# Performance work log

Measured on AMD Instinct MI355X. Metric: run time of the kernel, lower is better.

## Reference

```python
import jax, jax.numpy as jnp
import numpy as np
from jax import lax

B, N, NCAM, NLVL = 2, 65536, 5, 3
CIN, MID, OUT, PTSC = 256, 128, 128, 128
H, W = 64, 112
EPS = 1e-3


def setup_inputs() -> dict:
    ks = jax.random.split(jax.random.key(0), 8)
    f32 = jnp.float32
    img_feats = jax.random.normal(ks[0], (NLVL, B * NCAM, CIN, H, W), f32)
    # points roughly in front of the cameras (z ~ 15) so many project in-bounds
    pts_xyz = jax.random.normal(ks[1], (B, N, 3), f32) * 10.0 + jnp.array([0.0, 0.0, 15.0], f32)
    cam_ids = jnp.sort(jax.random.randint(ks[2], (B, N), 0, NCAM), axis=1).astype(jnp.int32)
    pts_feats = jax.random.normal(ks[3], (B * N, PTSC), f32)
    T = jnp.broadcast_to(jnp.eye(4, dtype=f32), (NCAM, 4, 4))
    T = T.at[:, :3, 3].set(jax.random.normal(ks[4], (NCAM, 3), f32) * 0.5)
    fx, fy, cx, cy = 400.0, 400.0, 4.0 * W, 4.0 * H  # full-res intrinsics (feature stride 8)
    K = jnp.broadcast_to(jnp.array([[fx, 0.0, cx], [0.0, fy, cy], [0.0, 0.0, 1.0]], f32), (NCAM, 3, 3))
    conv_w = jax.random.normal(ks[5], (NLVL, MID, CIN, 3, 3), f32) * 0.02
    conv_b = jnp.zeros((NLVL, MID), f32)
    img_w = jax.random.normal(ks[6], (OUT, MID * NLVL), f32) * 0.05
    img_b = jnp.zeros((OUT,), f32)
    img_gamma = jnp.ones((OUT,), f32)
    img_beta = jnp.zeros((OUT,), f32)
    pts_w = jax.random.normal(ks[7], (OUT, PTSC), f32) * 0.05
    pts_b = jnp.zeros((OUT,), f32)
    pts_gamma = jnp.ones((OUT,), f32)
    pts_beta = jnp.zeros((OUT,), f32)
    return dict(img_feats=img_feats, pts_xyz=pts_xyz, pts_feats=pts_feats, T=T, K=K,
                conv_w=conv_w, conv_b=conv_b, img_w=img_w, img_b=img_b,
                img_gamma=img_gamma, img_beta=img_beta, pts_w=pts_w, pts_b=pts_b,
                pts_gamma=pts_gamma, pts_beta=pts_beta, cam_ids=cam_ids)


def _bn(x, gamma, beta):
    # BatchNorm1d in training mode: batch statistics, biased variance, eps=1e-3
    mu = jnp.mean(x, axis=0)
    var = jnp.var(x, axis=0)
    return (x - mu) * lax.rsqrt(var + EPS) * gamma + beta


def _bilinear(feat, bidx, cam, px, py):
    # feat: [B, NCAM, H, W, C]; px/py: [B, N] pixel coords (align_corners=True)
    # grid_sample bilinear with zeros padding: out-of-bounds corners contribute 0
    x0f = jnp.floor(px)
    y0f = jnp.floor(py)
    wx1 = px - x0f
    wy1 = py - y0f

    def corner(xf, yf, wgt):
        valid = (xf >= 0) & (xf <= W - 1) & (yf >= 0) & (yf <= H - 1)
        xi = jnp.clip(xf, 0, W - 1).astype(jnp.int32)
        yi = jnp.clip(yf, 0, H - 1).astype(jnp.int32)
        v = feat[bidx, cam, yi, xi]  # [B, N, C]
        return v * (wgt * valid)[..., None]

    return (corner(x0f, y0f, (1 - wx1) * (1 - wy1))
            + corner(x0f + 1, y0f, wx1 * (1 - wy1))
            + corner(x0f, y0f + 1, (1 - wx1) * wy1)
            + corner(x0f + 1, y0f + 1, wx1 * wy1))


def _forward(img_feats, pts_xyz, pts_feats, T, K, conv_w, conv_b, img_w, img_b,
             img_gamma, img_beta, pts_w, pts_b, pts_gamma, pts_beta, cam_ids):
    # scale intrinsics to the 1/8-resolution feature maps (K[0,0],K[0,2],K[1,1],K[1,2] /= 8)
    k_scale = jnp.array([[0.125, 1.0, 0.125], [1.0, 0.125, 0.125], [1.0, 1.0, 1.0]], jnp.float32)
    Ks = K * k_scale
    ones = jnp.ones(pts_xyz.shape[:2] + (1,), pts_xyz.dtype)
    xyz1 = jnp.concatenate([pts_xyz, ones], axis=-1)      # [B, N, 4]
    Tc = T[cam_ids]                                        # [B, N, 4, 4]
    Kc = Ks[cam_ids]                                       # [B, N, 3, 3]
    pc = jnp.einsum('bnij,bnj->bni', Tc, xyz1)[..., :3]    # camera-frame coords
    pim = jnp.einsum('bnij,bnj->bni', Kc, pc)
    uv = pim[..., :2] / pim[..., 2:3]
    gx = uv[..., 0] / W * 2.0 - 1.0                        # normalized grid coords
    gy = uv[..., 1] / H * 2.0 - 1.0
    px = (gx + 1.0) * 0.5 * (W - 1)                        # align_corners=True mapping
    py = (gy + 1.0) * 0.5 * (H - 1)
    bidx = jnp.broadcast_to(jnp.arange(B)[:, None], cam_ids.shape)
    lvl_feats = []
    for l in range(NLVL):
        f = lax.conv_general_dilated(img_feats[l], conv_w[l], (1, 1), 'SAME',
                                     dimension_numbers=('NCHW', 'OIHW', 'NCHW'))
        f = f + conv_b[l][None, :, None, None]
        f = f.reshape(B, NCAM, MID, H, W).transpose(0, 1, 3, 4, 2)  # [B,NCAM,H,W,C]
        lvl_feats.append(_bilinear(f, bidx, cam_ids, px, py))       # [B,N,MID]
    img_pts = jnp.concatenate(lvl_feats, axis=-1).reshape(B * N, MID * NLVL)
    img_pre = _bn(img_pts @ img_w.T + img_b, img_gamma, img_beta)
    pts_pre = _bn(pts_feats @ pts_w.T + pts_b, pts_gamma, pts_beta)
    return jax.nn.relu(img_pre + pts_pre)


def reference(img_feats, pts_xyz, pts_feats, T, K, conv_w, conv_b, img_w, img_b,
              img_gamma, img_beta, pts_w, pts_b, pts_gamma, pts_beta, cam_ids):
    return _forward(img_feats, pts_xyz, pts_feats, T, K, conv_w, conv_b, img_w, img_b,
                    img_gamma, img_beta, pts_w, pts_b, pts_gamma, pts_beta, cam_ids)
```

## Files before the change

kernel.cpp:

```cpp
#include <hip/hip_runtime.h>
#include <cstdint>

#define LVLPOS 75240
#define GUARD  256
#define NPOST  75264

using f32x4  = __attribute__((ext_vector_type(4))) float;
using bf16x8 = __attribute__((ext_vector_type(8))) __bf16;

static __device__ __forceinline__ unsigned short f2bf(float f) {
  unsigned int u = __float_as_uint(f);
  u += 0x7fffu + ((u >> 16) & 1u);
  return (unsigned short)(u >> 16);
}
static __device__ __forceinline__ float bflo(uint32_t d) { return __uint_as_float(d << 16); }
static __device__ __forceinline__ float bfhi(uint32_t d) { return __uint_as_float(d & 0xffff0000u); }

#if __has_builtin(__builtin_amdgcn_global_load_lds)
#define HAVE_GLL 1
typedef const __attribute__((address_space(1))) unsigned int* gas1_t;
typedef __attribute__((address_space(3))) unsigned int* las3_t;
static __device__ __forceinline__ void gll16(const void* g, void* l) {
  __builtin_amdgcn_global_load_lds((gas1_t)g, (las3_t)l, 16, 0, 0);
}
#else
#define HAVE_GLL 0
#endif

#define OFF_WF     ((size_t)0)
#define OFF_BIAS   ((size_t)1769472)
#define OFF_PTSWB  ((size_t)1769984)
#define OFF_STATS  ((size_t)1802752)
#define OFF_FDAT   ((size_t)1804800)
#define OFF_IMGP   ((size_t)21072384)
#define OFF_IRAW   OFF_IMGP
#define OFF_PRAW   (OFF_IMGP + (size_t)33554432)

__global__ __launch_bounds__(256) void k_zero(unsigned short* __restrict__ imgP) {
  const int b = blockIdx.x, t = threadIdx.x;
  size_t base; int n16;
  if (b == 0)      { base = 0;                          n16 = 8192; }
  else if (b == 1) { base = (size_t)(GUARD + 3 * LVLPOS) * 256; n16 = 8192; }
  else {
    int z = b - 2, lvl = z / 20, w = z % 20, n = w >> 1, y = (w & 1) ? 65 : 0;
    base = (size_t)(GUARD + lvl * LVLPOS + (n * 66 + y) * 114) * 256;
    n16 = 3648;
  }
  uint4 zz = {0u, 0u, 0u, 0u};
  uint4* d = (uint4*)(imgP + base);
  for (int v = t; v < n16; v += 256) d[v] = zz;
}

__global__ __launch_bounds__(256) void k_fold_w(const float* __restrict__ img_w,
                                                const float* __restrict__ conv_w,
                                                unsigned short* __restrict__ wf) {
  __shared__ float iw[128 * 130];
  __shared__ float cw[128 * 33];
  const int bid = blockIdx.x;
  const int l = bid / 72, r = bid % 72, tap = r / 8, ckk = r % 8;
  const int t = threadIdx.x;
  for (int v = t; v < 4096; v += 256) {
    int o = v >> 5, seg = v & 31;
    float4 f = *(const float4*)(img_w + o * 384 + l * 128 + seg * 4);
    float* d = iw + o * 130 + seg * 4;
    d[0] = f.x; d[1] = f.y; d[2] = f.z; d[3] = f.w;
  }
  for (int v = t; v < 4096; v += 256) {
    int mid = v >> 5, cj = v & 31;
    cw[mid * 33 + cj] = conv_w[(size_t)(((l * 128 + mid) * 256) + (ckk * 32 + cj)) * 9 + tap];
  }
  __syncthreads();
  const int o = t & 127, cs = t >> 7;
  float accs[16];
  #pragma unroll
  for (int ci = 0; ci < 16; ++ci) accs[ci] = 0.f;
  for (int mid = 0; mid < 128; ++mid) {
    float a = iw[o * 130 + mid];
    #pragma unroll
    for (int ci = 0; ci < 16; ++ci) accs[ci] = fmaf(a, cw[mid * 33 + cs * 16 + ci], accs[ci]);
  }
  const int nt = o >> 4;
  #pragma unroll
  for (int ci = 0; ci < 16; ++ci) {
    int c = ckk * 32 + cs * 16 + ci;
    int ck64 = c >> 6, c64 = c & 63;
    int kh = c64 >> 5, kq3 = (c64 >> 3) & 3, el = c64 & 7;
    int lane = (o & 15) + (kq3 << 4);
    size_t idx = (size_t)((l * 4 + ck64) * 9 + tap) * 8192
               + (size_t)((nt * 2 + kh) * 512) + lane * 8 + el;
    wf[idx] = f2bf(accs[ci]);
  }
}

__global__ __launch_bounds__(256) void k_misc(const float* __restrict__ img_w,
                                              const float* __restrict__ conv_b,
                                              const float* __restrict__ pts_w,
                                              float* __restrict__ bias,
                                              unsigned short* __restrict__ pts_wb) {
  const int t = threadIdx.x;
  if (blockIdx.x == 0) {
    if (t < 128) {
      float a = 0.f;
      for (int i = 0; i < 384; ++i) a = fmaf(img_w[t * 384 + i], conv_b[i], a);
      bias[t] = a;
    }
  } else {
    int idx = (blockIdx.x - 1) * 256 + t;
    pts_wb[idx] = f2bf(pts_w[idx]);
  }
}

__global__ __launch_bounds__(256) void k_nhwc(const float* __restrict__ img,
                                              unsigned short* __restrict__ imgP) {
  __shared__ unsigned short tile[256 * 114];
  const int t = threadIdx.x;
  const int lvl = blockIdx.x / 640, r = blockIdx.x % 640, n = r >> 6, y = r & 63;
  const float4* src4 = (const float4*)(img + (size_t)(lvl * 10 + n) * 1835008 + (size_t)y * 112);
  for (int v = t; v < 7168; v += 256) {
    int c = v / 28, s = v - c * 28;
    float4 f = src4[(size_t)c * 1792 + s];
    uint2 d;
    d.x = (uint32_t)f2bf(f.x) | ((uint32_t)f2bf(f.y) << 16);
    d.y = (uint32_t)f2bf(f.z) | ((uint32_t)f2bf(f.w) << 16);
    *(uint2*)(tile + c * 114 + s * 4) = d;
  }
  __syncthreads();
  uint32_t* dst = (uint32_t*)(imgP + (size_t)(GUARD + lvl * LVLPOS + (n * 66 + y + 1) * 114) * 256);
  for (int v = t; v < 14592; v += 256) {
    int xp = v >> 7, cp = v & 127;
    uint32_t val = 0;
    if (xp >= 1 && xp <= 112) {
      int x = xp - 1;
      val = (uint32_t)tile[(2 * cp) * 114 + x] | ((uint32_t)tile[(2 * cp + 1) * 114 + x] << 16);
    }
    dst[v] = val;
  }
}

__global__ __launch_bounds__(256, 3) void k_conv(const unsigned short* __restrict__ imgP,
                                                 const unsigned short* __restrict__ wf,
                                                 const float* __restrict__ bias,
                                                 unsigned short* __restrict__ fdat) {
  __shared__ unsigned short lds[9360 + 2 * 8192];
  unsigned short* As = lds;
  unsigned short* Bs = lds + 9360;
  const int t = threadIdx.x, lane = t & 63, wave = t >> 6;
  const int mh = wave & 1, nh = wave >> 1;
  const int m = lane & 15, kq = lane >> 4;
  const int m0 = blockIdx.x * 128;

  f32x4 acc[4][4];
  #pragma unroll
  for (int i = 0; i < 4; ++i)
    #pragma unroll
    for (int j = 0; j < 4; ++j) acc[i][j] = (f32x4){0.f, 0.f, 0.f, 0.f};

  for (int lvl = 0; lvl < 3; ++lvl) {
    const unsigned short* Alvl = imgP + ((size_t)GUARD + (size_t)lvl * LVLPOS + m0 - 1) * 256;
    for (int ck = 0; ck < 4; ++ck) {
      for (int ky = 0; ky < 3; ++ky) {
        const unsigned short* Asrc = Alvl + (ptrdiff_t)(ky - 1) * 114 * 256 + ck * 64;
        for (int v = t; v < 1040; v += 256) {
          int p = v >> 3, seg = v & 7;
          uint4 d = *(const uint4*)(Asrc + (size_t)p * 256 + seg * 8);
          *(uint4*)(As + p * 72 + seg * 8) = d;
        }
        const unsigned short* Bsrc = wf + (size_t)((lvl * 4 + ck) * 9 + ky * 3) * 8192;
#if HAVE_GLL
        #pragma unroll
        for (int i = 0; i < 4; ++i) {
          int chunk = wave * 4 + i;
          gll16(Bsrc + chunk * 512 + lane * 8, Bs + chunk * 512);
        }
#else
        for (int v = t; v < 1024; v += 256)
          *(uint4*)(Bs + v * 8) = *(const uint4*)(Bsrc + v * 8);
#endif
        __syncthreads();
        #pragma unroll
        for (int kx = 0; kx < 3; ++kx) {
          if (kx < 2) {
            const unsigned short* Bn = Bsrc + (kx + 1) * 8192;
            unsigned short* Bd = Bs + ((kx + 1) & 1) * 8192;
#if HAVE_GLL
            #pragma unroll
            for (int i = 0; i < 4; ++i) {
              int chunk = wave * 4 + i;
              gll16(Bn + chunk * 512 + lane * 8, Bd + chunk * 512);
            }
#else
            for (int v = t; v < 1024; v += 256)
              *(uint4*)(Bd + v * 8) = *(const uint4*)(Bn + v * 8);
#endif
          }
          const unsigned short* Bb = Bs + (kx & 1) * 8192;
          bf16x8 bfr[4][2];
          #pragma unroll
          for (int nt = 0; nt < 4; ++nt) {
            const unsigned short* bp = Bb + ((nh * 4 + nt) * 2) * 512 + lane * 8;
            bfr[nt][0] = *(const bf16x8*)(bp);
            bfr[nt][1] = *(const bf16x8*)(bp + 512);
          }
          #pragma unroll
          for (int mt = 0; mt < 4; ++mt) {
            const unsigned short* ap = As + (mh * 64 + mt * 16 + m + kx) * 72 + kq * 8;
            bf16x8 a0 = *(const bf16x8*)(ap);
            bf16x8 a1 = *(const bf16x8*)(ap + 32);
            #pragma unroll
            for (int nt = 0; nt < 4; ++nt) {
              acc[mt][nt] = __builtin_amdgcn_mfma_f32_16x16x32_bf16(a0, bfr[nt][0], acc[mt][nt], 0, 0, 0);
              acc[mt][nt] = __builtin_amdgcn_mfma_f32_16x16x32_bf16(a1, bfr[nt][1], acc[mt][nt], 0, 0, 0);
            }
          }
          __syncthreads();
        }
      }
    }
  }

  unsigned short* Ep = lds;
  #pragma unroll
  for (int nt = 0; nt < 4; ++nt) {
    int oc = nh * 64 + nt * 16 + m;
    float bv = bias[oc];
    #pragma unroll
    for (int mt = 0; mt < 4; ++mt)
      #pragma unroll
      for (int rr = 0; rr < 4; ++rr)
        Ep[(mh * 64 + mt * 16 + kq * 4 + rr) * 128 + oc] = f2bf(acc[mt][nt][rr] + bv);
  }
  __syncthreads();
  unsigned short* dst = fdat + (size_t)m0 * 128;
  for (int v = t; v < 2048; v += 256)
    *(uint4*)(dst + v * 8) = *(const uint4*)(Ep + v * 8);
}

__global__ __launch_bounds__(256) void k_gather(const float* __restrict__ pts_xyz,
                                                const int* __restrict__ cam_ids,
                                                const float* __restrict__ Tm,
                                                const float* __restrict__ Km,
                                                const unsigned short* __restrict__ fdat,
                                                unsigned short* __restrict__ img_raw) {
  const int t = threadIdx.x, lane = t & 63, wave = t >> 6;
  const int p0 = blockIdx.x * 16 + wave * 4;
  const uint32_t* fq = (const uint32_t*)fdat;
  for (int j = 0; j < 4; ++j) {
    const int p = p0 + j;
    const int b = p >> 16;
    const int cam = cam_ids[p];
    const float X = pts_xyz[(size_t)p * 3], Y = pts_xyz[(size_t)p * 3 + 1], Z = pts_xyz[(size_t)p * 3 + 2];
    const float* Tc = Tm + cam * 16;
    float pcx = Tc[0] * X + Tc[1] * Y + Tc[2]  * Z + Tc[3];
    float pcy = Tc[4] * X + Tc[5] * Y + Tc[6]  * Z + Tc[7];
    float pcz = Tc[8] * X + Tc[9] * Y + Tc[10] * Z + Tc[11];
    const float* Kc = Km + cam * 9;
    float pimx = Kc[0] * 0.125f * pcx + Kc[1] * pcy          + Kc[2] * 0.125f * pcz;
    float pimy = Kc[3] * pcx          + Kc[4] * 0.125f * pcy + Kc[5] * 0.125f * pcz;
    float pimz = Kc[6] * pcx          + Kc[7] * pcy          + Kc[8] * pcz;
    float u = pimx / pimz, vv = pimy / pimz;
    float px = (u / 112.f) * 111.f;
    float py = (vv / 64.f) * 63.f;
    float x0 = floorf(px), y0 = floorf(py);
    float wx = px - x0, wy = py - y0;
    float cxf[4] = {x0, x0 + 1.f, x0, x0 + 1.f};
    float cyf[4] = {y0, y0, y0 + 1.f, y0 + 1.f};
    float cwt[4] = {(1.f - wx) * (1.f - wy), wx * (1.f - wy), (1.f - wx) * wy, wx * wy};
    const int nimg = b * 5 + cam;
    float wv[4]; int idx[4]; bool any = false;
    #pragma unroll
    for (int c4 = 0; c4 < 4; ++c4) {
      float xf = cxf[c4], yf = cyf[c4];
      bool valid = (xf >= 0.f) && (xf <= 111.f) && (yf >= 0.f) && (yf <= 63.f);
      float w = cwt[c4] * (valid ? 1.f : 0.f);
      int xi = (int)fminf(fmaxf(xf, 0.f), 111.f);
      int yi = (int)fminf(fmaxf(yf, 0.f), 63.f);
      wv[c4] = w;
      idx[c4] = (nimg * 66 + yi + 1) * 114 + xi + 1;
      any = any || (w != 0.f);
    }
    float acc0 = 0.f, acc1 = 0.f;
    if (any) {
      #pragma unroll
      for (int c4 = 0; c4 < 4; ++c4) {
        uint32_t d = fq[(size_t)idx[c4] * 64 + lane];
        acc0 = fmaf(wv[c4], bflo(d), acc0);
        acc1 = fmaf(wv[c4], bfhi(d), acc1);
      }
    }
    ((uint32_t*)img_raw)[(size_t)p * 64 + lane] =
        (uint32_t)f2bf(acc0) | ((uint32_t)f2bf(acc1) << 16);
  }
}

#define PP 136
__global__ __launch_bounds__(256, 2) void k_ptsgemm(const float* __restrict__ pts_feats,
                                                    const unsigned short* __restrict__ pts_wb,
                                                    unsigned short* __restrict__ pts_raw) {
  __shared__ unsigned short Asm[128 * PP];
  __shared__ unsigned short Bsm[128 * PP];
  const int t = threadIdx.x, lane = t & 63, wave = t >> 6;
  const int mh = wave & 1, nh = wave >> 1;
  const int m = lane & 15, kq = lane >> 4;
  const size_t r0 = (size_t)blockIdx.x * 128;
  for (int v = t; v < 2048; v += 256) {
    int o = v >> 4, seg = v & 15;
    *(uint4*)(Bsm + o * PP + seg * 8) = *(const uint4*)(pts_wb + o * 128 + seg * 8);
  }
  for (int v = t; v < 4096; v += 256) {
    int mm = v >> 5, seg = v & 31;
    float4 f = *(const float4*)(pts_feats + (r0 + mm) * 128 + seg * 4);
    uint2 d;
    d.x = (uint32_t)f2bf(f.x) | ((uint32_t)f2bf(f.y) << 16);
    d.y = (uint32_t)f2bf(f.z) | ((uint32_t)f2bf(f.w) << 16);
    *(uint2*)(Asm + mm * PP + seg * 4) = d;
  }
  __syncthreads();
  f32x4 acc[4][4];
  #pragma unroll
  for (int i = 0; i < 4; ++i)
    #pragma unroll
    for (int jj = 0; jj < 4; ++jj) acc[i][jj] = (f32x4){0.f, 0.f, 0.f, 0.f};
  #pragma unroll
  for (int ks = 0; ks < 4; ++ks) {
    bf16x8 bfr[4];
    #pragma unroll
    for (int nt = 0; nt < 4; ++nt)
      bfr[nt] = *(const bf16x8*)(Bsm + (nh * 64 + nt * 16 + m) * PP + ks * 32 + kq * 8);
    #pragma unroll
    for (int mt = 0; mt < 4; ++mt) {
      bf16x8 af = *(const bf16x8*)(Asm + (mh * 64 + mt * 16 + m) * PP + ks * 32 + kq * 8);
      #pragma unroll
      for (int nt = 0; nt < 4; ++nt)
        acc[mt][nt] = __builtin_amdgcn_mfma_f32_16x16x32_bf16(af, bfr[nt], acc[mt][nt], 0, 0, 0);
    }
  }
  __syncthreads();
  #pragma unroll
  for (int mt = 0; mt < 4; ++mt)
    #pragma unroll
    for (int nt = 0; nt < 4; ++nt)
      #pragma unroll
      for (int rr = 0; rr < 4; ++rr)
        Asm[(mh * 64 + mt * 16 + kq * 4 + rr) * 128 + nh * 64 + nt * 16 + m] = f2bf(acc[mt][nt][rr]);
  __syncthreads();
  unsigned short* dst = pts_raw + r0 * 128;
  for (int v = t; v < 2048; v += 256)
    *(uint4*)(dst + v * 8) = *(const uint4*)(Asm + v * 8);
}

__global__ __launch_bounds__(256) void k_stats(const unsigned short* __restrict__ img_raw,
                                               const unsigned short* __restrict__ pts_raw,
                                               float* __restrict__ stats) {
  const int bid = blockIdx.x;
  const uint32_t* src = (const uint32_t*)((bid < 256) ? img_raw : pts_raw);
  const int blk = bid & 255;
  const int t = threadIdx.x, cp = t & 63, rg = t >> 6;
  float s0 = 0.f, q0 = 0.f, s1 = 0.f, q1 = 0.f;
  for (int i = 0; i < 128; ++i) {
    int row = blk * 512 + rg * 128 + i;
    uint32_t d = src[(size_t)row * 64 + cp];
    float v0 = bflo(d), v1 = bfhi(d);
    s0 += v0; q0 += v0 * v0; s1 += v1; q1 += v1 * v1;
  }
  const int base = (bid < 256) ? 0 : 256;
  atomicAdd(&stats[base + 2 * cp], s0);
  atomicAdd(&stats[base + 2 * cp + 1], s1);
  atomicAdd(&stats[base + 128 + 2 * cp], q0);
  atomicAdd(&stats[base + 128 + 2 * cp + 1], q1);
}

__global__ __launch_bounds__(256) void k_final(const unsigned short* __restrict__ img_raw,
                                               const unsigned short* __restrict__ pts_raw,
                                               const float* __restrict__ stats,
                                               const float* __restrict__ img_gamma,
                                               const float* __restrict__ img_beta,
                                               const float* __restrict__ pts_gamma,
                                               const float* __restrict__ pts_beta,
                                               float* __restrict__ out) {
  __shared__ float sA[128], sB[128], sC[128];
  const int t = threadIdx.x;
  if (t < 128) {
    const float Nr = 131072.f;
    float mu_i = stats[t] / Nr;
    float var_i = stats[128 + t] / Nr - mu_i * mu_i;
    float a_i = img_gamma[t] * rsqrtf(var_i + 1e-3f);
    float mu_p = stats[256 + t] / Nr;
    float var_p = stats[384 + t] / Nr - mu_p * mu_p;
    float a_p = pts_gamma[t] * rsqrtf(var_p + 1e-3f);
    sA[t] = a_i; sB[t] = a_p;
    sC[t] = img_beta[t] + pts_beta[t] - a_i * mu_i - a_p * mu_p;
  }
  __syncthreads();
  const uint32_t* ir = (const uint32_t*)img_raw;
  const uint32_t* pr = (const uint32_t*)pts_raw;
  size_t g0 = (size_t)blockIdx.x * 2048;
  for (int i = 0; i < 8; ++i) {
    size_t g = g0 + i * 256 + t;
    uint32_t di = ir[g], dp = pr[g];
    int c = (int)(g & 63) * 2;
    float o0 = fmaxf(0.f, sA[c] * bflo(di) + sB[c] * bflo(dp) + sC[c]);
    float o1 = fmaxf(0.f, sA[c + 1] * bfhi(di) + sB[c + 1] * bfhi(dp) + sC[c + 1]);
    float2 o; o.x = o0; o.y = o1;
    *(float2*)(out + g * 2) = o;
  }
}

extern "C" void kernel_launch(void* const* d_in, const int* in_sizes, int n_in,
                              void* d_out, int out_size, void* d_ws, size_t ws_size,
                              hipStream_t stream) {
  const float* img_feats = (const float*)d_in[0];
  const float* pts_xyz   = (const float*)d_in[1];
  const float* pts_feats = (const float*)d_in[2];
  const float* Tm        = (const float*)d_in[3];
  const float* Km        = (const float*)d_in[4];
  const float* conv_w    = (const float*)d_in[5];
  const float* conv_b    = (const float*)d_in[6];
  const float* img_w     = (const float*)d_in[7];
  const float* img_gamma = (const float*)d_in[9];
  const float* img_beta  = (const float*)d_in[10];
  const float* pts_w     = (const float*)d_in[11];
  const float* pts_gamma = (const float*)d_in[13];
  const float* pts_beta  = (const float*)d_in[14];
  const int*   cam_ids   = (const int*)d_in[15];

  char* wsb = (char*)d_ws;
  unsigned short* wf      = (unsigned short*)(wsb + OFF_WF);
  float*          bias    = (float*)(wsb + OFF_BIAS);
  unsigned short* pts_wb  = (unsigned short*)(wsb + OFF_PTSWB);
  float*          stats   = (float*)(wsb + OFF_STATS);
  unsigned short* fdat    = (unsigned short*)(wsb + OFF_FDAT);
  unsigned short* imgP    = (unsigned short*)(wsb + OFF_IMGP);
  unsigned short* img_raw = (unsigned short*)(wsb + OFF_IRAW);
  unsigned short* pts_raw = (unsigned short*)(wsb + OFF_PRAW);

  hipMemsetAsync(stats, 0, 2048, stream);
  k_zero<<<dim3(62), dim3(256), 0, stream>>>(imgP);
  k_fold_w<<<dim3(216), dim3(256), 0, stream>>>(img_w, conv_w, wf);
  k_misc<<<dim3(65), dim3(256), 0, stream>>>(img_w, conv_b, pts_w, bias, pts_wb);

  k_nhwc<<<dim3(1920), dim3(256), 0, stream>>>(img_feats, imgP);
  k_conv<<<dim3(588), dim3(256), 0, stream>>>(imgP, wf, bias, fdat);

  k_gather<<<dim3(8192), dim3(256), 0, stream>>>(pts_xyz, cam_ids, Tm, Km, fdat, img_raw);
  k_ptsgemm<<<dim3(1024), dim3(256), 0, stream>>>(pts_feats, pts_wb, pts_raw);
  k_stats<<<dim3(512), dim3(256), 0, stream>>>(img_raw, pts_raw, stats);
  k_final<<<dim3(4096), dim3(256), 0, stream>>>(img_raw, pts_raw, stats,
                                                img_gamma, img_beta, pts_gamma, pts_beta,
                                                (float*)d_out);
}
```

Measured before the change: 753.9 us.

## Merge setup kernels, retile conv, fuse gather with pts GEMM and stats

```diff
diff --git a/kernel.cpp b/kernel.cpp
--- a/kernel.cpp
+++ b/kernel.cpp
@@ -3,7 +3,7 @@
 
 #define LVLPOS 75240
 #define GUARD  256
-#define NPOST  75264
+#define NPART  16
 
 using f32x4  = __attribute__((ext_vector_type(4))) float;
 using bf16x8 = __attribute__((ext_vector_type(8))) __bf16;
@@ -16,97 +16,90 @@
 static __device__ __forceinline__ float bflo(uint32_t d) { return __uint_as_float(d << 16); }
 static __device__ __forceinline__ float bfhi(uint32_t d) { return __uint_as_float(d & 0xffff0000u); }
 
-#if __has_builtin(__builtin_amdgcn_global_load_lds)
-#define HAVE_GLL 1
-typedef const __attribute__((address_space(1))) unsigned int* gas1_t;
-typedef __attribute__((address_space(3))) unsigned int* las3_t;
-static __device__ __forceinline__ void gll16(const void* g, void* l) {
-  __builtin_amdgcn_global_load_lds((gas1_t)g, (las3_t)l, 16, 0, 0);
-}
-#else
-#define HAVE_GLL 0
-#endif
-
 #define OFF_WF     ((size_t)0)
 #define OFF_BIAS   ((size_t)1769472)
 #define OFF_PTSWB  ((size_t)1769984)
-#define OFF_STATS  ((size_t)1802752)
-#define OFF_FDAT   ((size_t)1804800)
-#define OFF_IMGP   ((size_t)21072384)
+#define OFF_STATSP ((size_t)1802752)
+#define OFF_FDAT   ((size_t)1835520)
+#define OFF_IMGP   ((size_t)21103104)
 #define OFF_IRAW   OFF_IMGP
 #define OFF_PRAW   (OFF_IMGP + (size_t)33554432)
 
-__global__ __launch_bounds__(256) void k_zero(unsigned short* __restrict__ imgP) {
+__global__ __launch_bounds__(256) void k_setup(const float* __restrict__ img_w,
+                                               const float* __restrict__ conv_w,
+                                               const float* __restrict__ conv_b,
+                                               const float* __restrict__ pts_w,
+                                               unsigned short* __restrict__ wf,
+                                               float* __restrict__ bias,
+                                               unsigned short* __restrict__ pts_wb,
+                                               unsigned short* __restrict__ imgP,
+                                               float* __restrict__ statsP) {
+  __shared__ float smem[12544];
   const int b = blockIdx.x, t = threadIdx.x;
-  size_t base; int n16;
-  if (b == 0)      { base = 0;                          n16 = 8192; }
-  else if (b == 1) { base = (size_t)(GUARD + 3 * LVLPOS) * 256; n16 = 8192; }
-  else {
-    int z = b - 2, lvl = z / 20, w = z % 20, n = w >> 1, y = (w & 1) ? 65 : 0;
-    base = (size_t)(GUARD + lvl * LVLPOS + (n * 66 + y) * 114) * 256;
-    n16 = 3648;
-  }
-  uint4 zz = {0u, 0u, 0u, 0u};
-  uint4* d = (uint4*)(imgP + base);
-  for (int v = t; v < n16; v += 256) d[v] = zz;
-}
-
-__global__ __launch_bounds__(256) void k_fold_w(const float* __restrict__ img_w,
-                                                const float* __restrict__ conv_w,
-                                                unsigned short* __restrict__ wf) {
-  __shared__ float iw[128 * 130];
-  __shared__ float cw[128 * 33];
-  const int bid = blockIdx.x;
-  const int l = bid / 72, r = bid % 72, tap = r / 8, ckk = r % 8;
-  const int t = threadIdx.x;
-  for (int v = t; v < 4096; v += 256) {
-    int o = v >> 5, seg = v & 31;
-    float4 f = *(const float4*)(img_w + o * 384 + l * 128 + seg * 4);
-    float* d = iw + o * 130 + seg * 4;
-    d[0] = f.x; d[1] = f.y; d[2] = f.z; d[3] = f.w;
-  }
-  for (int v = t; v < 4096; v += 256) {
-    int mid = v >> 5, cj = v & 31;
-    cw[mid * 33 + cj] = conv_w[(size_t)(((l * 128 + mid) * 256) + (ckk * 32 + cj)) * 9 + tap];
-  }
-  __syncthreads();
-  const int o = t & 127, cs = t >> 7;
-  float accs[16];
-  #pragma unroll
-  for (int ci = 0; ci < 16; ++ci) accs[ci] = 0.f;
-  for (int mid = 0; mid < 128; ++mid) {
-    float a = iw[o * 130 + mid];
-    #pragma unroll
-    for (int ci = 0; ci < 16; ++ci) accs[ci] = fmaf(a, cw[mid * 33 + cs * 16 + ci], accs[ci]);
-  }
-  const int nt = o >> 4;
-  #pragma unroll
-  for (int ci = 0; ci < 16; ++ci) {
-    int c = ckk * 32 + cs * 16 + ci;
-    int ck64 = c >> 6, c64 = c & 63;
-    int kh = c64 >> 5, kq3 = (c64 >> 3) & 3, el = c64 & 7;
-    int lane = (o & 15) + (kq3 << 4);
-    size_t idx = (size_t)((l * 4 + ck64) * 9 + tap) * 8192
-               + (size_t)((nt * 2 + kh) * 512) + lane * 8 + el;
-    wf[idx] = f2bf(accs[ci]);
-  }
-}
-
-__global__ __launch_bounds__(256) void k_misc(const float* __restrict__ img_w,
-                                              const float* __restrict__ conv_b,
-                                              const float* __restrict__ pts_w,
-                                              float* __restrict__ bias,
-                                              unsigned short* __restrict__ pts_wb) {
-  const int t = threadIdx.x;
-  if (blockIdx.x == 0) {
-    if (t < 128) {
-      float a = 0.f;
-      for (int i = 0; i < 384; ++i) a = fmaf(img_w[t * 384 + i], conv_b[i], a);
-      bias[t] = a;
+  if (b < 432) {
+    int z = b >> 1, oh = b & 1;
+    int l = z / 72, r = z % 72, tap = r / 8, ckk = r % 8;
+    float* iw = smem;
+    float* cw = smem + 8320;
+    for (int v = t; v < 2048; v += 256) {
+      int o = v >> 5, seg = v & 31;
+      float4 f = *(const float4*)(img_w + (size_t)(oh * 64 + o) * 384 + l * 128 + seg * 4);
+      float* d = iw + o * 130 + seg * 4;
+      d[0] = f.x; d[1] = f.y; d[2] = f.z; d[3] = f.w;
+    }
+    for (int v = t; v < 4096; v += 256) {
+      int mid = v >> 5, cj = v & 31;
+      cw[mid * 33 + cj] = conv_w[(size_t)((l * 128 + mid) * 256 + ckk * 32 + cj) * 9 + tap];
+    }
+    __syncthreads();
+    const int o64 = t & 63, cs = t >> 6, o = oh * 64 + o64;
+    float accs[8];
+    #pragma unroll
+    for (int ci = 0; ci < 8; ++ci) accs[ci] = 0.f;
+    for (int mid = 0; mid < 128; ++mid) {
+      float a = iw[o64 * 130 + mid];
+      #pragma unroll
+      for (int ci = 0; ci < 8; ++ci) accs[ci] = fmaf(a, cw[mid * 33 + cs * 8 + ci], accs[ci]);
+    }
+    #pragma unroll
+    for (int ci = 0; ci < 8; ++ci) {
+      int c = ckk * 32 + cs * 8 + ci;
+      int ck64 = c >> 6, c64 = c & 63;
+      int kh = c64 >> 5, kq3 = (c64 >> 3) & 3, el = c64 & 7;
+      size_t idx = (size_t)((l * 4 + ck64) * 9 + tap) * 8192
+                 + (size_t)(((o >> 4) * 2 + kh) * 512) + ((o & 15) + 16 * kq3) * 8 + el;
+      wf[idx] = f2bf(accs[ci]);
+    }
+  } else if (b < 494) {
+    int z = b - 432;
+    size_t base; int n16;
+    if (z == 60)      { base = 0; n16 = 8192; }
+    else if (z == 61) { base = (size_t)(GUARD + 3 * LVLPOS) * 256; n16 = 8192; }
+    else {
+      int lvl = z / 20, w = z % 20, n = w >> 1, y = (w & 1) ? 65 : 0;
+      base = (size_t)(GUARD + lvl * LVLPOS + (n * 66 + y) * 114) * 256; n16 = 3648;
+    }
+    uint4 zz = {0u, 0u, 0u, 0u};
+    uint4* d = (uint4*)(imgP + base);
+    for (int v = t; v < n16; v += 256) d[v] = zz;
+  } else if (b < 559) {
+    int z = b - 494;
+    if (z == 0) {
+      if (t < 128) {
+        float a = 0.f;
+        for (int i = 0; i < 384; ++i) a = fmaf(img_w[t * 384 + i], conv_b[i], a);
+        bias[t] = a;
+      }
+    } else {
+      int idx = (z - 1) * 256 + t;
+      int o = idx >> 7, k = idx & 127;
+      int ks = k >> 5, kq = (k >> 3) & 3, el = k & 7;
+      int pos = (ks * 8 + (o >> 4)) * 512 + ((o & 15) + 16 * kq) * 8 + el;
+      pts_wb[pos] = f2bf(pts_w[idx]);
     }
   } else {
-    int idx = (blockIdx.x - 1) * 256 + t;
-    pts_wb[idx] = f2bf(pts_w[idx]);
+    int z = b - 559;
+    ((float4*)statsP)[z * 256 + t] = (float4){0.f, 0.f, 0.f, 0.f};
   }
 }
 
@@ -137,241 +130,242 @@
   }
 }
 
-__global__ __launch_bounds__(256, 3) void k_conv(const unsigned short* __restrict__ imgP,
+#define APITCH 72
+static __device__ __forceinline__ void conv_stage(unsigned short* dst,
+                                                  const unsigned short* __restrict__ imgP,
+                                                  int s, int m0, int t) {
+  int lvl = s / 12, r = s - lvl * 12;
+  int ck = r / 3, ky = r - ck * 3;
+  const unsigned short* base = imgP
+      + (size_t)(GUARD + lvl * LVLPOS + m0 - 1 + (ky - 1) * 114) * 256 + ck * 64;
+  for (int v = t; v < 528; v += 256) {
+    int p = v >> 3, seg = v & 7;
+    *(uint4*)(dst + p * APITCH + seg * 8) = *(const uint4*)(base + (size_t)p * 256 + seg * 8);
+  }
+}
+
+static __device__ __forceinline__ void conv_compute(const unsigned short* As_,
+                                                    const unsigned short* __restrict__ wf,
+                                                    int s, int mh, int nh, int m, int kq,
+                                                    f32x4 (&acc)[2][4]) {
+  const unsigned short* W0 = wf + (size_t)(3 * s) * 8192 + (nh * 8) * 512 + (m + 16 * kq) * 8;
+  #pragma unroll
+  for (int kx = 0; kx < 3; ++kx) {
+    const unsigned short* Wp = W0 + kx * 8192;
+    bf16x8 bv[4][2];
+    #pragma unroll
+    for (int nt = 0; nt < 4; ++nt) {
+      bv[nt][0] = *(const bf16x8*)(Wp + (nt * 2) * 512);
+      bv[nt][1] = *(const bf16x8*)(Wp + (nt * 2 + 1) * 512);
+    }
+    #pragma unroll
+    for (int mt = 0; mt < 2; ++mt) {
+      const unsigned short* ap = As_ + (mh * 32 + mt * 16 + m + kx) * APITCH + kq * 8;
+      bf16x8 a0 = *(const bf16x8*)(ap);
+      bf16x8 a1 = *(const bf16x8*)(ap + 32);
+      #pragma unroll
+      for (int nt = 0; nt < 4; ++nt) {
+        acc[mt][nt] = __builtin_amdgcn_mfma_f32_16x16x32_bf16(a0, bv[nt][0], acc[mt][nt], 0, 0, 0);
+        acc[mt][nt] = __builtin_amdgcn_mfma_f32_16x16x32_bf16(a1, bv[nt][1], acc[mt][nt], 0, 0, 0);
+      }
+    }
+  }
+}
+
+__global__ __launch_bounds__(256, 4) void k_conv(const unsigned short* __restrict__ imgP,
                                                  const unsigned short* __restrict__ wf,
                                                  const float* __restrict__ bias,
                                                  unsigned short* __restrict__ fdat) {
-  __shared__ unsigned short lds[9360 + 2 * 8192];
-  unsigned short* As = lds;
-  unsigned short* Bs = lds + 9360;
+  __shared__ unsigned short As[2][66 * APITCH];
   const int t = threadIdx.x, lane = t & 63, wave = t >> 6;
   const int mh = wave & 1, nh = wave >> 1;
   const int m = lane & 15, kq = lane >> 4;
-  const int m0 = blockIdx.x * 128;
-
-  f32x4 acc[4][4];
+  const int m0 = blockIdx.x * 64;
+
+  f32x4 acc[2][4];
   #pragma unroll
-  for (int i = 0; i < 4; ++i)
+  for (int i = 0; i < 2; ++i)
     #pragma unroll
     for (int j = 0; j < 4; ++j) acc[i][j] = (f32x4){0.f, 0.f, 0.f, 0.f};
 
-  for (int lvl = 0; lvl < 3; ++lvl) {
-    const unsigned short* Alvl = imgP + ((size_t)GUARD + (size_t)lvl * LVLPOS + m0 - 1) * 256;
-    for (int ck = 0; ck < 4; ++ck) {
-      for (int ky = 0; ky < 3; ++ky) {
-        const unsigned short* Asrc = Alvl + (ptrdiff_t)(ky - 1) * 114 * 256 + ck * 64;
-        for (int v = t; v < 1040; v += 256) {
-          int p = v >> 3, seg = v & 7;
-          uint4 d = *(const uint4*)(Asrc + (size_t)p * 256 + seg * 8);
-          *(uint4*)(As + p * 72 + seg * 8) = d;
-        }
-        const unsigned short* Bsrc = wf + (size_t)((lvl * 4 + ck) * 9 + ky * 3) * 8192;
-#if HAVE_GLL
-        #pragma unroll
-        for (int i = 0; i < 4; ++i) {
-          int chunk = wave * 4 + i;
-          gll16(Bsrc + chunk * 512 + lane * 8, Bs + chunk * 512);
-        }
-#else
-        for (int v = t; v < 1024; v += 256)
-          *(uint4*)(Bs + v * 8) = *(const uint4*)(Bsrc + v * 8);
-#endif
-        __syncthreads();
-        #pragma unroll
-        for (int kx = 0; kx < 3; ++kx) {
-          if (kx < 2) {
-            const unsigned short* Bn = Bsrc + (kx + 1) * 8192;
-            unsigned short* Bd = Bs + ((kx + 1) & 1) * 8192;
-#if HAVE_GLL
-            #pragma unroll
-            for (int i = 0; i < 4; ++i) {
-              int chunk = wave * 4 + i;
-              gll16(Bn + chunk * 512 + lane * 8, Bd + chunk * 512);
-            }
-#else
-            for (int v = t; v < 1024; v += 256)
-              *(uint4*)(Bd + v * 8) = *(const uint4*)(Bn + v * 8);
-#endif
-          }
-          const unsigned short* Bb = Bs + (kx & 1) * 8192;
-          bf16x8 bfr[4][2];
-          #pragma unroll
-          for (int nt = 0; nt < 4; ++nt) {
-            const unsigned short* bp = Bb + ((nh * 4 + nt) * 2) * 512 + lane * 8;
-            bfr[nt][0] = *(const bf16x8*)(bp);
-            bfr[nt][1] = *(const bf16x8*)(bp + 512);
-          }
-          #pragma unroll
-          for (int mt = 0; mt < 4; ++mt) {
-            const unsigned short* ap = As + (mh * 64 + mt * 16 + m + kx) * 72 + kq * 8;
-            bf16x8 a0 = *(const bf16x8*)(ap);
-            bf16x8 a1 = *(const bf16x8*)(ap + 32);
-            #pragma unroll
-            for (int nt = 0; nt < 4; ++nt) {
-              acc[mt][nt] = __builtin_amdgcn_mfma_f32_16x16x32_bf16(a0, bfr[nt][0], acc[mt][nt], 0, 0, 0);
-              acc[mt][nt] = __builtin_amdgcn_mfma_f32_16x16x32_bf16(a1, bfr[nt][1], acc[mt][nt], 0, 0, 0);
-            }
-          }
-          __syncthreads();
-        }
-      }
-    }
-  }
-
-  unsigned short* Ep = lds;
+  conv_stage(As[0], imgP, 0, m0, t);
+  #pragma unroll 1
+  for (int s = 0; s < 36; s += 2) {
+    __syncthreads();
+    if (s + 1 < 36) conv_stage(As[1], imgP, s + 1, m0, t);
+    conv_compute(As[0], wf, s, mh, nh, m, kq, acc);
+    __syncthreads();
+    if (s + 2 < 36) conv_stage(As[0], imgP, s + 2, m0, t);
+    conv_compute(As[1], wf, s + 1, mh, nh, m, kq, acc);
+  }
+  __syncthreads();
+
+  unsigned short* Ep = &As[0][0];
   #pragma unroll
   for (int nt = 0; nt < 4; ++nt) {
     int oc = nh * 64 + nt * 16 + m;
     float bv = bias[oc];
     #pragma unroll
-    for (int mt = 0; mt < 4; ++mt)
+    for (int mt = 0; mt < 2; ++mt)
       #pragma unroll
       for (int rr = 0; rr < 4; ++rr)
-        Ep[(mh * 64 + mt * 16 + kq * 4 + rr) * 128 + oc] = f2bf(acc[mt][nt][rr] + bv);
+        Ep[(mh * 32 + mt * 16 + kq * 4 + rr) * 128 + oc] = f2bf(acc[mt][nt][rr] + bv);
   }
   __syncthreads();
   unsigned short* dst = fdat + (size_t)m0 * 128;
-  for (int v = t; v < 2048; v += 256)
+  for (int v = t; v < 1024; v += 256)
     *(uint4*)(dst + v * 8) = *(const uint4*)(Ep + v * 8);
 }
 
-__global__ __launch_bounds__(256) void k_gather(const float* __restrict__ pts_xyz,
-                                                const int* __restrict__ cam_ids,
-                                                const float* __restrict__ Tm,
-                                                const float* __restrict__ Km,
-                                                const unsigned short* __restrict__ fdat,
-                                                unsigned short* __restrict__ img_raw) {
+__global__ __launch_bounds__(256) void k_gp(const float* __restrict__ pts_xyz,
+                                            const int* __restrict__ cam_ids,
+                                            const float* __restrict__ Tm,
+                                            const float* __restrict__ Km,
+                                            const unsigned short* __restrict__ fdat,
+                                            const float* __restrict__ pts_feats,
+                                            const unsigned short* __restrict__ pts_wb,
+                                            unsigned short* __restrict__ img_raw,
+                                            unsigned short* __restrict__ pts_raw,
+                                            float* __restrict__ statsP) {
+  __shared__ __align__(16) char smem[36864];
   const int t = threadIdx.x, lane = t & 63, wave = t >> 6;
-  const int p0 = blockIdx.x * 16 + wave * 4;
-  const uint32_t* fq = (const uint32_t*)fdat;
-  for (int j = 0; j < 4; ++j) {
-    const int p = p0 + j;
-    const int b = p >> 16;
-    const int cam = cam_ids[p];
-    const float X = pts_xyz[(size_t)p * 3], Y = pts_xyz[(size_t)p * 3 + 1], Z = pts_xyz[(size_t)p * 3 + 2];
-    const float* Tc = Tm + cam * 16;
-    float pcx = Tc[0] * X + Tc[1] * Y + Tc[2]  * Z + Tc[3];
-    float pcy = Tc[4] * X + Tc[5] * Y + Tc[6]  * Z + Tc[7];
-    float pcz = Tc[8] * X + Tc[9] * Y + Tc[10] * Z + Tc[11];
-    const float* Kc = Km + cam * 9;
-    float pimx = Kc[0] * 0.125f * pcx + Kc[1] * pcy          + Kc[2] * 0.125f * pcz;
-    float pimy = Kc[3] * pcx          + Kc[4] * 0.125f * pcy + Kc[5] * 0.125f * pcz;
-    float pimz = Kc[6] * pcx          + Kc[7] * pcy          + Kc[8] * pcz;
-    float u = pimx / pimz, vv = pimy / pimz;
-    float px = (u / 112.f) * 111.f;
-    float py = (vv / 64.f) * 63.f;
-    float x0 = floorf(px), y0 = floorf(py);
-    float wx = px - x0, wy = py - y0;
-    float cxf[4] = {x0, x0 + 1.f, x0, x0 + 1.f};
-    float cyf[4] = {y0, y0, y0 + 1.f, y0 + 1.f};
-    float cwt[4] = {(1.f - wx) * (1.f - wy), wx * (1.f - wy), (1.f - wx) * wy, wx * wy};
-    const int nimg = b * 5 + cam;
-    float wv[4]; int idx[4]; bool any = false;
-    #pragma unroll
-    for (int c4 = 0; c4 < 4; ++c4) {
-      float xf = cxf[c4], yf = cyf[c4];
-      bool valid = (xf >= 0.f) && (xf <= 111.f) && (yf >= 0.f) && (yf <= 63.f);
-      float w = cwt[c4] * (valid ? 1.f : 0.f);
-      int xi = (int)fminf(fmaxf(xf, 0.f), 111.f);
-      int yi = (int)fminf(fmaxf(yf, 0.f), 63.f);
-      wv[c4] = w;
-      idx[c4] = (nimg * 66 + yi + 1) * 114 + xi + 1;
-      any = any || (w != 0.f);
-    }
-    float acc0 = 0.f, acc1 = 0.f;
-    if (any) {
+
+  if (blockIdx.x < 8192) {
+    float* sb = (float*)smem;
+    float* qb = sb + 128;
+    if (t < 128) { sb[t] = 0.f; sb[128 + t] = 0.f; }
+    __syncthreads();
+    const int p0 = blockIdx.x * 16 + wave * 4;
+    const uint32_t* fq = (const uint32_t*)fdat;
+    float s0 = 0.f, q0 = 0.f, s1 = 0.f, q1 = 0.f;
+    for (int j = 0; j < 4; ++j) {
+      const int p = p0 + j;
+      const int b = p >> 16;
+      const int cam = cam_ids[p];
+      const float X = pts_xyz[(size_t)p * 3], Y = pts_xyz[(size_t)p * 3 + 1], Z = pts_xyz[(size_t)p * 3 + 2];
+      const float* Tc = Tm + cam * 16;
+      float pcx = Tc[0] * X + Tc[1] * Y + Tc[2]  * Z + Tc[3];
+      float pcy = Tc[4] * X + Tc[5] * Y + Tc[6]  * Z + Tc[7];
+      float pcz = Tc[8] * X + Tc[9] * Y + Tc[10] * Z + Tc[11];
+      const float* Kc = Km + cam * 9;
+      float pimx = Kc[0] * 0.125f * pcx + Kc[1] * pcy          + Kc[2] * 0.125f * pcz;
+      float pimy = Kc[3] * pcx          + Kc[4] * 0.125f * pcy + Kc[5] * 0.125f * pcz;
+      float pimz = Kc[6] * pcx          + Kc[7] * pcy          + Kc[8] * pcz;
+      float u = pimx / pimz, vv = pimy / pimz;
+      float px = (u / 112.f) * 111.f;
+      float py = (vv / 64.f) * 63.f;
+      float x0 = floorf(px), y0 = floorf(py);
+      float wx = px - x0, wy = py - y0;
+      float cxf[4] = {x0, x0 + 1.f, x0, x0 + 1.f};
+      float cyf[4] = {y0, y0, y0 + 1.f, y0 + 1.f};
+      float cwt[4] = {(1.f - wx) * (1.f - wy), wx * (1.f - wy), (1.f - wx) * wy, wx * wy};
+      const int nimg = b * 5 + cam;
+      float wv[4]; int idx[4]; bool any = false;
       #pragma unroll
       for (int c4 = 0; c4 < 4; ++c4) {
-        uint32_t d = fq[(size_t)idx[c4] * 64 + lane];
-        acc0 = fmaf(wv[c4], bflo(d), acc0);
-        acc1 = fmaf(wv[c4], bfhi(d), acc1);
-      }
-    }
-    ((uint32_t*)img_raw)[(size_t)p * 64 + lane] =
-        (uint32_t)f2bf(acc0) | ((uint32_t)f2bf(acc1) << 16);
-  }
-}
-
-#define PP 136
-__global__ __launch_bounds__(256, 2) void k_ptsgemm(const float* __restrict__ pts_feats,
-                                                    const unsigned short* __restrict__ pts_wb,
-                                                    unsigned short* __restrict__ pts_raw) {
-  __shared__ unsigned short Asm[128 * PP];
-  __shared__ unsigned short Bsm[128 * PP];
-  const int t = threadIdx.x, lane = t & 63, wave = t >> 6;
-  const int mh = wave & 1, nh = wave >> 1;
-  const int m = lane & 15, kq = lane >> 4;
-  const size_t r0 = (size_t)blockIdx.x * 128;
-  for (int v = t; v < 2048; v += 256) {
-    int o = v >> 4, seg = v & 15;
-    *(uint4*)(Bsm + o * PP + seg * 8) = *(const uint4*)(pts_wb + o * 128 + seg * 8);
-  }
-  for (int v = t; v < 4096; v += 256) {
-    int mm = v >> 5, seg = v & 31;
-    float4 f = *(const float4*)(pts_feats + (r0 + mm) * 128 + seg * 4);
-    uint2 d;
-    d.x = (uint32_t)f2bf(f.x) | ((uint32_t)f2bf(f.y) << 16);
-    d.y = (uint32_t)f2bf(f.z) | ((uint32_t)f2bf(f.w) << 16);
-    *(uint2*)(Asm + mm * PP + seg * 4) = d;
-  }
-  __syncthreads();
-  f32x4 acc[4][4];
-  #pragma unroll
-  for (int i = 0; i < 4; ++i)
-    #pragma unroll
-    for (int jj = 0; jj < 4; ++jj) acc[i][jj] = (f32x4){0.f, 0.f, 0.f, 0.f};
-  #pragma unroll
-  for (int ks = 0; ks < 4; ++ks) {
-    bf16x8 bfr[4];
-    #pragma unroll
-    for (int nt = 0; nt < 4; ++nt)
-      bfr[nt] = *(const bf16x8*)(Bsm + (nh * 64 + nt * 16 + m) * PP + ks * 32 + kq * 8);
-    #pragma unroll
-    for (int mt = 0; mt < 4; ++mt) {
-      bf16x8 af = *(const bf16x8*)(Asm + (mh * 64 + mt * 16 + m) * PP + ks * 32 + kq * 8);
+        float xf = cxf[c4], yf = cyf[c4];
+        bool valid = (xf >= 0.f) && (xf <= 111.f) && (yf >= 0.f) && (yf <= 63.f);
+        float w = cwt[c4] * (valid ? 1.f : 0.f);
+        int xi = (int)fminf(fmaxf(xf, 0.f), 111.f);
+        int yi = (int)fminf(fmaxf(yf, 0.f), 63.f);
+        wv[c4] = w;
+        idx[c4] = (nimg * 66 + yi + 1) * 114 + xi + 1;
+        any = any || (w != 0.f);
+      }
+      float a0 = 0.f, a1 = 0.f;
+      if (any) {
+        #pragma unroll
+        for (int c4 = 0; c4 < 4; ++c4) {
+          uint32_t d = fq[(size_t)idx[c4] * 64 + lane];
+          a0 = fmaf(wv[c4], bflo(d), a0);
+          a1 = fmaf(wv[c4], bfhi(d), a1);
+        }
+      }
+      s0 += a0; q0 += a0 * a0; s1 += a1; q1 += a1 * a1;
+      ((uint32_t*)img_raw)[(size_t)p * 64 + lane] =
+          (uint32_t)f2bf(a0) | ((uint32_t)f2bf(a1) << 16);
+    }
+    atomicAdd(&sb[lane * 2], s0);
+    atomicAdd(&sb[lane * 2 + 1], s1);
+    atomicAdd(&qb[lane * 2], q0);
+    atomicAdd(&qb[lane * 2 + 1], q1);
+    __syncthreads();
+    if (t < 128) {
+      float* sp = statsP + (size_t)(blockIdx.x & (NPART - 1)) * 512;
+      atomicAdd(sp + t, sb[t]);
+      atomicAdd(sp + 128 + t, qb[t]);
+    }
+  } else {
+    const int pb = blockIdx.x - 8192;
+    const size_t r0 = (size_t)pb * 128;
+    unsigned short* As2 = (unsigned short*)smem;
+    const int mh = wave & 1, nh = wave >> 1;
+    const int m = lane & 15, kq = lane >> 4;
+    for (int v = t; v < 4096; v += 256) {
+      int mm = v >> 5, seg = v & 31;
+      float4 f = *(const float4*)(pts_feats + (r0 + mm) * 128 + seg * 4);
+      uint2 d;
+      d.x = (uint32_t)f2bf(f.x) | ((uint32_t)f2bf(f.y) << 16);
+      d.y = (uint32_t)f2bf(f.z) | ((uint32_t)f2bf(f.w) << 16);
+      *(uint2*)(As2 + mm * 136 + seg * 4) = d;
+    }
+    __syncthreads();
+    f32x4 acc[4][4];
+    #pragma unroll
+    for (int i = 0; i < 4; ++i)
+      #pragma unroll
+      for (int jj = 0; jj < 4; ++jj) acc[i][jj] = (f32x4){0.f, 0.f, 0.f, 0.f};
+    #pragma unroll
+    for (int ks = 0; ks < 4; ++ks) {
+      bf16x8 bv[4];
       #pragma unroll
       for (int nt = 0; nt < 4; ++nt)
-        acc[mt][nt] = __builtin_amdgcn_mfma_f32_16x16x32_bf16(af, bfr[nt], acc[mt][nt], 0, 0, 0);
-    }
-  }
-  __syncthreads();
-  #pragma unroll
-  for (int mt = 0; mt < 4; ++mt)
-    #pragma unroll
-    for (int nt = 0; nt < 4; ++nt)
-      #pragma unroll
-      for (int rr = 0; rr < 4; ++rr)
-        Asm[(mh * 64 + mt * 16 + kq * 4 + rr) * 128 + nh * 64 + nt * 16 + m] = f2bf(acc[mt][nt][rr]);
-  __syncthreads();
-  unsigned short* dst = pts_raw + r0 * 128;
-  for (int v = t; v < 2048; v += 256)
-    *(uint4*)(dst + v * 8) = *(const uint4*)(Asm + v * 8);
-}
-
-__global__ __launch_bounds__(256) void k_stats(const unsigned short* __restrict__ img_raw,
-                                               const unsigned short* __restrict__ pts_raw,
-                                               float* __restrict__ stats) {
-  const int bid = blockIdx.x;
-  const uint32_t* src = (const uint32_t*)((bid < 256) ? img_raw : pts_raw);
-  const int blk = bid & 255;
-  const int t = threadIdx.x, cp = t & 63, rg = t >> 6;
-  float s0 = 0.f, q0 = 0.f, s1 = 0.f, q1 = 0.f;
-  for (int i = 0; i < 128; ++i) {
-    int row = blk * 512 + rg * 128 + i;
-    uint32_t d = src[(size_t)row * 64 + cp];
-    float v0 = bflo(d), v1 = bfhi(d);
-    s0 += v0; q0 += v0 * v0; s1 += v1; q1 += v1 * v1;
-  }
-  const int base = (bid < 256) ? 0 : 256;
-  atomicAdd(&stats[base + 2 * cp], s0);
-  atomicAdd(&stats[base + 2 * cp + 1], s1);
-  atomicAdd(&stats[base + 128 + 2 * cp], q0);
-  atomicAdd(&stats[base + 128 + 2 * cp + 1], q1);
+        bv[nt] = *(const bf16x8*)(pts_wb + (size_t)((ks * 8 + nh * 4 + nt) * 512) + lane * 8);
+      #pragma unroll
+      for (int mt = 0; mt < 4; ++mt) {
+        bf16x8 af = *(const bf16x8*)(As2 + (mh * 64 + mt * 16 + m) * 136 + ks * 32 + kq * 8);
+        #pragma unroll
+        for (int nt = 0; nt < 4; ++nt)
+          acc[mt][nt] = __builtin_amdgcn_mfma_f32_16x16x32_bf16(af, bv[nt], acc[mt][nt], 0, 0, 0);
+      }
+    }
+    __syncthreads();
+    #pragma unroll
+    for (int mt = 0; mt < 4; ++mt)
+      #pragma unroll
+      for (int nt = 0; nt < 4; ++nt)
+        #pragma unroll
+        for (int rr = 0; rr < 4; ++rr)
+          As2[(mh * 64 + mt * 16 + kq * 4 + rr) * 128 + nh * 64 + nt * 16 + m] = f2bf(acc[mt][nt][rr]);
+    __syncthreads();
+    unsigned short* dst = pts_raw + r0 * 128;
+    for (int v = t; v < 2048; v += 256)
+      *(uint4*)(dst + v * 8) = *(const uint4*)(As2 + v * 8);
+    float* ps = (float*)(smem + 34816);
+    float* pq = ps + 256;
+    pq = (float*)(smem + 35840);
+    {
+      int col = t & 127, rh = t >> 7;
+      float s = 0.f, q = 0.f;
+      for (int i = 0; i < 64; ++i) {
+        float v = __uint_as_float((uint32_t)As2[(rh * 64 + i) * 128 + col] << 16);
+        s += v; q += v * v;
+      }
+      ps[rh * 128 + col] = s;
+      pq[rh * 128 + col] = q;
+    }
+    __syncthreads();
+    if (t < 128) {
+      float* sp = statsP + (size_t)(blockIdx.x & (NPART - 1)) * 512;
+      atomicAdd(sp + 256 + t, ps[t] + ps[128 + t]);
+      atomicAdd(sp + 384 + t, pq[t] + pq[128 + t]);
+    }
+  }
 }
 
 __global__ __launch_bounds__(256) void k_final(const unsigned short* __restrict__ img_raw,
                                                const unsigned short* __restrict__ pts_raw,
-                                               const float* __restrict__ stats,
+                                               const float* __restrict__ statsP,
                                                const float* __restrict__ img_gamma,
                                                const float* __restrict__ img_beta,
                                                const float* __restrict__ pts_gamma,
@@ -380,12 +374,17 @@
   __shared__ float sA[128], sB[128], sC[128];
   const int t = threadIdx.x;
   if (t < 128) {
+    float si = 0.f, qi = 0.f, sp = 0.f, qp = 0.f;
+    for (int k = 0; k < NPART; ++k) {
+      const float* st = statsP + (size_t)k * 512;
+      si += st[t]; qi += st[128 + t]; sp += st[256 + t]; qp += st[384 + t];
+    }
     const float Nr = 131072.f;
-    float mu_i = stats[t] / Nr;
-    float var_i = stats[128 + t] / Nr - mu_i * mu_i;
+    float mu_i = si / Nr;
+    float var_i = qi / Nr - mu_i * mu_i;
     float a_i = img_gamma[t] * rsqrtf(var_i + 1e-3f);
-    float mu_p = stats[256 + t] / Nr;
-    float var_p = stats[384 + t] / Nr - mu_p * mu_p;
+    float mu_p = sp / Nr;
+    float var_p = qp / Nr - mu_p * mu_p;
     float a_p = pts_gamma[t] * rsqrtf(var_p + 1e-3f);
     sA[t] = a_i; sB[t] = a_p;
     sC[t] = img_beta[t] + pts_beta[t] - a_i * mu_i - a_p * mu_p;
@@ -427,24 +426,19 @@
   unsigned short* wf      = (unsigned short*)(wsb + OFF_WF);
   float*          bias    = (float*)(wsb + OFF_BIAS);
   unsigned short* pts_wb  = (unsigned short*)(wsb + OFF_PTSWB);
-  float*          stats   = (float*)(wsb + OFF_STATS);
+  float*          statsP  = (float*)(wsb + OFF_STATSP);
   unsigned short* fdat    = (unsigned short*)(wsb + OFF_FDAT);
   unsigned short* imgP    = (unsigned short*)(wsb + OFF_IMGP);
   unsigned short* img_raw = (unsigned short*)(wsb + OFF_IRAW);
   unsigned short* pts_raw = (unsigned short*)(wsb + OFF_PRAW);
 
-  hipMemsetAsync(stats, 0, 2048, stream);
-  k_zero<<<dim3(62), dim3(256), 0, stream>>>(imgP);
-  k_fold_w<<<dim3(216), dim3(256), 0, stream>>>(img_w, conv_w, wf);
-  k_misc<<<dim3(65), dim3(256), 0, stream>>>(img_w, conv_b, pts_w, bias, pts_wb);
-
+  k_setup<<<dim3(567), dim3(256), 0, stream>>>(img_w, conv_w, conv_b, pts_w,
+                                               wf, bias, pts_wb, imgP, statsP);
   k_nhwc<<<dim3(1920), dim3(256), 0, stream>>>(img_feats, imgP);
-  k_conv<<<dim3(588), dim3(256), 0, stream>>>(imgP, wf, bias, fdat);
-
-  k_gather<<<dim3(8192), dim3(256), 0, stream>>>(pts_xyz, cam_ids, Tm, Km, fdat, img_raw);
-  k_ptsgemm<<<dim3(1024), dim3(256), 0, stream>>>(pts_feats, pts_wb, pts_raw);
-  k_stats<<<dim3(512), dim3(256), 0, stream>>>(img_raw, pts_raw, stats);
-  k_final<<<dim3(4096), dim3(256), 0, stream>>>(img_raw, pts_raw, stats,
+  k_conv<<<dim3(1176), dim3(256), 0, stream>>>(imgP, wf, bias, fdat);
+  k_gp<<<dim3(9216), dim3(256), 0, stream>>>(pts_xyz, cam_ids, Tm, Km, fdat,
+                                             pts_feats, pts_wb, img_raw, pts_raw, statsP);
+  k_final<<<dim3(4096), dim3(256), 0, stream>>>(img_raw, pts_raw, statsP,
                                                 img_gamma, img_beta, pts_gamma, pts_beta,
                                                 (float*)d_out);
 }
```

Result: no change. 742.3 us (-1.5%).
